# Kernel optimization log

Hardware: AMD Instinct MI355X
Metric: run time of the kernel (lower is better)

Reference implementation:

```python
import jax, jax.numpy as jnp
import numpy as np

BN_EPS = 1e-5

def _bn(x, gamma, beta):
    # BatchNorm1d in training mode: batch mean, biased variance
    m = jnp.mean(x, axis=0)
    v = jnp.var(x, axis=0)
    return (x - m) * jax.lax.rsqrt(v + BN_EPS) * gamma + beta

def setup_inputs() -> dict:
    key = jax.random.key(0)
    ks = jax.random.split(key, 12)
    N, E, D, ED = 50000, 600000, 128, 16
    s = lambda k, sh: jax.random.normal(k, sh, dtype=jnp.float32) * 0.05
    return {
        'h': jax.random.normal(ks[0], (N, D), dtype=jnp.float32),
        'edge_index': jax.random.randint(ks[1], (2, E), 0, N, dtype=jnp.int64),
        'edge_attr': jax.random.normal(ks[2], (E, ED), dtype=jnp.float32),
        'ee_w1': s(ks[3], (ED, D)), 'ee_b1': jnp.zeros((D,), jnp.float32),
        'ee_g1': jnp.ones((D,), jnp.float32), 'ee_bb1': jnp.zeros((D,), jnp.float32),
        'ee_w2': s(ks[4], (D, D)), 'ee_b2': jnp.zeros((D,), jnp.float32),
        'mlp_w1': s(ks[5], (D, D)), 'mlp_b1': jnp.zeros((D,), jnp.float32),
        'mlp_g1': jnp.ones((D,), jnp.float32), 'mlp_bb1': jnp.zeros((D,), jnp.float32),
        'mlp_w2': s(ks[6], (D, D)), 'mlp_b2': jnp.zeros((D,), jnp.float32),
        'mlp_g2': jnp.ones((D,), jnp.float32), 'mlp_bb2': jnp.zeros((D,), jnp.float32),
    }

def reference(h, edge_index, edge_attr, ee_w1, ee_b1, ee_g1, ee_bb1, ee_w2, ee_b2,
              mlp_w1, mlp_b1, mlp_g1, mlp_bb1, mlp_w2, mlp_b2, mlp_g2, mlp_bb2):
    N = h.shape[0]
    src, dst = edge_index[0], edge_index[1]
    # edge_encoder: Linear -> BN -> ReLU -> Linear
    e = jax.nn.relu(_bn(edge_attr @ ee_w1 + ee_b1, ee_g1, ee_bb1)) @ ee_w2 + ee_b2  # [E, D]
    # scatter-add edge embeddings to destination nodes
    agg_edge = jax.ops.segment_sum(e, dst, num_segments=N)  # [N, D]
    h = h + agg_edge
    # GINConv (eps=0): mlp(h + sum_{j->i} h_j)
    neigh = jax.ops.segment_sum(h[src], dst, num_segments=N)  # [N, D]
    z = h + neigh
    z = jax.nn.relu(_bn(z @ mlp_w1 + mlp_b1, mlp_g1, mlp_bb1))
    z = jax.nn.relu(_bn(z @ mlp_w2 + mlp_b2, mlp_g2, mlp_bb2))
    return z
```

## Files before the change

kernel.cpp:

```cpp
#include <hip/hip_runtime.h>
#include <hip/hip_bf16.h>

#define DD 128
#define EDIM 16
#define WPB 4
#define PSE 68
#define NCOPY 16
#define PREP_TB 208
#define PREP_AM 1024
#define PREP_HI 1024

typedef short v8s __attribute__((ext_vector_type(8)));
typedef float v4f __attribute__((ext_vector_type(4)));

__device__ __forceinline__ float ldf(const void* p, int i, int bf){
  return bf ? __bfloat162float(((const __hip_bfloat16*)p)[i])
            : ((const float*)p)[i];
}
__device__ __forceinline__ float bfu_lo(unsigned u){
  unsigned b = (u & 0xffffu) << 16; float f; __builtin_memcpy(&f,&b,4); return f;
}
__device__ __forceinline__ float bfu_hi(unsigned u){
  unsigned b = u & 0xffff0000u; float f; __builtin_memcpy(&f,&b,4); return f;
}
__device__ __forceinline__ unsigned short f2bf(float f){
  unsigned u; __builtin_memcpy(&u,&f,4);
  unsigned r = (u + 0x7fffu + ((u>>16)&1u)) >> 16;
  return (unsigned short)r;
}
__device__ __forceinline__ unsigned packbf(float a, float b){
  return (unsigned)f2bf(a) | ((unsigned)f2bf(b) << 16);
}

__global__ void k_detect(const void* g1, const int* ei, int E, int* flags){
  __shared__ int nz;
  if (threadIdx.x==0) nz = 0;
  __syncthreads();
  long long total = 2LL*E;
  long long stride = (total/1024) & ~1LL;
  if (stride < 2) stride = 2;
  long long idx = (long long)threadIdx.x*stride + 1;
  if (idx < total && ei[idx] != 0) atomicAdd(&nz, 1);
  __syncthreads();
  if (threadIdx.x==0){
    unsigned w = *(const unsigned*)g1;
    flags[0] = (w == 0x3F803F80u) ? 1 : 0;
    flags[1] = (nz == 0) ? 1 : 0;
  }
}

__global__ __launch_bounds__(256) void k_prep(
    const void* w0, const void* w1, const void* w2, const void* we1,
    const void* __restrict__ attr, const int* __restrict__ ei, int E,
    const int* __restrict__ flags, short* __restrict__ Bt,
    float* __restrict__ Ssum, float* __restrict__ csum, int* __restrict__ deg)
{
  const int b = blockIdx.x;
  const int t = threadIdx.x;
  if (b < PREP_TB){
    const int bf = flags[0];
    for (int idx = b*256 + t; idx < 3*16384 + 2048; idx += PREP_TB*256){
      if (idx < 3*16384){
        int m = idx >> 14, r = idx & 16383;
        int nn = r >> 7, k = r & 127;
        const void* w = (m==0) ? w0 : ((m==1) ? w1 : w2);
        Bt[idx] = (short)f2bf(ldf(w, k*DD + nn, bf));
      } else {
        int r = idx - 3*16384;
        int nn = r >> 4, k = r & 15;
        Bt[idx] = (short)f2bf(ldf(we1, k*DD + nn, bf));
      }
    }
    return;
  }
  if (b < PREP_TB + PREP_AM){
    const int rb = b - PREP_TB;
    __shared__ short Ws[4*512];
    __shared__ float sred[4][256];
    __shared__ float credu[4][16];
    const int wv = t >> 6, lane = t & 63, l15 = lane & 15, quad = lane >> 4;
    const int bf = flags[0];
    const int el = lane >> 1, half = lane & 1;
    short* W = &Ws[wv*512];

    v4f acc = (v4f){0.f,0.f,0.f,0.f};
    float cs[8];
    #pragma unroll
    for (int j=0;j<8;++j) cs[j]=0.f;

    const int nchunks = (E + 31) >> 5;
    for (int c = rb*4 + wv; c < nchunks; c += PREP_AM*4){
      const int e = c*32 + el;
      const bool ok = (e < E);
      float f[8];
      if (bf){
        uint4 u = {0u,0u,0u,0u};
        if (ok) u = reinterpret_cast<const uint4*>(attr)[(size_t)e*2 + half];
        f[0]=bfu_lo(u.x); f[1]=bfu_hi(u.x); f[2]=bfu_lo(u.y); f[3]=bfu_hi(u.y);
        f[4]=bfu_lo(u.z); f[5]=bfu_hi(u.z); f[6]=bfu_lo(u.w); f[7]=bfu_hi(u.w);
      } else {
        float4 v0 = {0,0,0,0}, v1 = {0,0,0,0};
        if (ok){
          const float4* ap = reinterpret_cast<const float4*>(attr) +
                             (size_t)e*4 + half*2;
          v0 = ap[0]; v1 = ap[1];
        }
        f[0]=v0.x; f[1]=v0.y; f[2]=v0.z; f[3]=v0.w;
        f[4]=v1.x; f[5]=v1.y; f[6]=v1.z; f[7]=v1.w;
      }
      #pragma unroll
      for (int j=0;j<8;++j){
        cs[j] += f[j];
        W[(half*8 + j)*32 + el] = (short)f2bf(f[j]);
      }
      v8s a = *reinterpret_cast<const v8s*>(&W[l15*32 + quad*8]);
      acc = __builtin_amdgcn_mfma_f32_16x16x32_bf16(a, a, acc, 0,0,0);
    }

    #pragma unroll
    for (int r=0;r<4;++r) sred[wv][(quad*4 + r)*16 + l15] = acc[r];
    #pragma unroll
    for (int j=0;j<8;++j){
      #pragma unroll
      for (int off=2; off<64; off<<=1) cs[j] += __shfl_xor(cs[j], off, 64);
    }
    if (lane < 2){
      #pragma unroll
      for (int j=0;j<8;++j) credu[wv][lane*8 + j] = cs[j];
    }
    __syncthreads();
    const int cp = rb & (NCOPY-1);
    float s = sred[0][t]+sred[1][t]+sred[2][t]+sred[3][t];
    atomicAdd(&Ssum[cp*256 + t], s);
    if (t < 16){
      float s2 = credu[0][t]+credu[1][t]+credu[2][t]+credu[3][t];
      atomicAdd(&csum[cp*16 + t], s2);
    }
    return;
  }
  {
    const int rb = b - (PREP_TB + PREP_AM);
    const int i64 = flags[1];
    const int2* ei2 = (const int2*)ei;
    for (int e = rb*256 + t; e < E; e += PREP_HI*256){
      int d = i64 ? ei2[E + e].x : ei[E + e];
      atomicAdd(&deg[d], 1);
    }
  }
}

__global__ __launch_bounds__(256) void k_scan_pe(
    const int* __restrict__ deg, int n, int nb,
    const void* __restrict__ w1, const void* __restrict__ g,
    const void* __restrict__ bb,
    const float* __restrict__ Ssum, const float* __restrict__ csum,
    float Einv, const int* __restrict__ flags,
    float* __restrict__ sc, float* __restrict__ sh,
    int* __restrict__ bsum)
{
  const int t = threadIdx.x;
  if ((int)blockIdx.x == nb){
    __shared__ float fS[256];
    __shared__ float fc[16];
    const int bf = flags[0];
    {
      float a0 = 0.f;
      #pragma unroll
      for (int c=0;c<NCOPY;++c) a0 += Ssum[c*256 + t];
      fS[t] = a0;
      if (t < 16){
        float a2 = 0.f;
        #pragma unroll
        for (int c=0;c<NCOPY;++c) a2 += csum[c*16 + t];
        fc[t] = a2;
      }
    }
    __syncthreads();
    if (t < 128){
      const int j = t;
      float w[EDIM];
      #pragma unroll
      for (int p=0;p<EDIM;++p) w[p] = ldf(w1, p*DD + j, bf);
      float mu0 = 0.f;
      #pragma unroll
      for (int p=0;p<EDIM;++p) mu0 += fc[p]*Einv*w[p];
      float s2 = 0.f;
      #pragma unroll
      for (int p=0;p<EDIM;++p){
        float acc = 0.f;
        #pragma unroll
        for (int q=0;q<EDIM;++q) acc += fS[p*16 + q]*w[q];
        s2 += w[p]*acc;
      }
      float var = s2*Einv - mu0*mu0;
      float scv = ldf(g, j, bf) * rsqrtf(var + 1e-5f);
      sc[j] = scv;
      sh[j] = ldf(bb, j, bf) - mu0*scv;
    }
    return;
  }
  __shared__ int red[256];
  const int base = blockIdx.x*1024;
  int s = 0;
  for (int i = t; i < 1024; i += 256){
    int gi = base + i;
    s += (gi < n) ? deg[gi] : 0;
  }
  red[t] = s; __syncthreads();
  for (int off=128; off>0; off>>=1){
    if (t < off) red[t] += red[t+off];
    __syncthreads();
  }
  if (t==0) bsum[blockIdx.x] = red[0];
}

__global__ void k_scan_final(const int* __restrict__ deg, int n, int nwin, int nb,
                             const int* __restrict__ bsum,
                             int* __restrict__ offsets, int* __restrict__ cursor,
                             int* __restrict__ win2node){
  __shared__ int red[256];
  __shared__ int pre[2];
  const int t = threadIdx.x;
  {
    int v = (t < nb) ? bsum[t] : 0;
    red[t] = v; __syncthreads();
    for (int off=1; off<256; off<<=1){
      int x = (t>=off) ? red[t-off] : 0;
      __syncthreads();
      red[t] += x; __syncthreads();
    }
    if (t == (int)blockIdx.x) pre[0] = red[t] - v;
    if (t == 255) pre[1] = red[255];
    __syncthreads();
  }
  const int base = blockIdx.x*1024 + t*4;
  int v4[4]; int s = 0;
  #pragma unroll
  for (int k=0;k<4;++k){
    int gi = base + k;
    v4[k] = (gi < n) ? deg[gi] : 0;
    s += v4[k];
  }
  red[t] = s; __syncthreads();
  for (int off=1; off<256; off<<=1){
    int x = (t>=off) ? red[t-off] : 0;
    __syncthreads();
    red[t] += x; __syncthreads();
  }
  int ex = pre[0] + red[t] - s;
  #pragma unroll
  for (int k=0;k<4;++k){
    int gi = base + k;
    if (gi < n){
      offsets[gi] = ex; cursor[gi] = ex;
      int end = ex + v4[k];
      for (int w = (ex + 63) >> 6; (w << 6) < end; ++w) win2node[w] = gi;
    }
    ex += v4[k];
  }
  if (blockIdx.x==0 && t==0){
    offsets[n] = pre[1];
    win2node[nwin] = n - 1;
  }
}

__global__ void k_scatter(const int* __restrict__ ei, int E,
                          const int* __restrict__ flags,
                          int* __restrict__ cursor, int2* __restrict__ se){
  const int i64 = flags[1];
  const int2* ei2 = (const int2*)ei;
  for (int e = blockIdx.x*blockDim.x + threadIdx.x; e < E;
       e += gridDim.x*blockDim.x){
    int d = i64 ? ei2[E + e].x : ei[E + e];
    int s = i64 ? ei2[e].x     : ei[e];
    int pp = atomicAdd(&cursor[d], 1);
    se[pp] = make_int2(s, e);
  }
}

__global__ __launch_bounds__(256) void k_edgeagg(
    const void* __restrict__ attr, const int2* __restrict__ se,
    const short* __restrict__ w1t,
    const float* __restrict__ sc, const float* __restrict__ sh,
    const int* __restrict__ offsets, const int* __restrict__ win2node,
    const int* __restrict__ flags, int n, int E, float* __restrict__ Pagg)
{
  __shared__ __align__(16) float Ps[DD*PSE];
  const int t = threadIdx.x;
  const int wv = t >> 6, lane = t & 63, l15 = lane & 15, quad = lane >> 4;
  const int bf = flags[0];
  const int G0 = blockIdx.x * (64*WPB);
  if (G0 >= E) return;

  const int4 w2nv = *reinterpret_cast<const int4*>(&win2node[blockIdx.x*WPB]);
  const int w2na[4] = {w2nv.x, w2nv.y, w2nv.z, w2nv.w};
  const int w2next = win2node[blockIdx.x*WPB + WPB];

  v8s afrag[WPB];
  #pragma unroll
  for (int w=0; w<WPB; ++w){
    afrag[w] = (v8s){0,0,0,0,0,0,0,0};
    if (quad < 2){
      int slot = G0 + w*64 + wv*16 + l15;
      if (slot < E){
        int e = se[slot].y;
        if (bf){
          afrag[w] = *reinterpret_cast<const v8s*>(
                (const short*)attr + (size_t)e*EDIM + quad*8);
        } else {
          const float4* ap = reinterpret_cast<const float4*>(
                (const float*)attr + (size_t)e*EDIM + quad*8);
          float4 v0 = ap[0], v1 = ap[1];
          v8s av;
          av[0]=(short)f2bf(v0.x); av[1]=(short)f2bf(v0.y);
          av[2]=(short)f2bf(v0.z); av[3]=(short)f2bf(v0.w);
          av[4]=(short)f2bf(v1.x); av[5]=(short)f2bf(v1.y);
          av[6]=(short)f2bf(v1.z); av[7]=(short)f2bf(v1.w);
          afrag[w] = av;
        }
      }
    }
  }

  v8s bfrag[8];
  #pragma unroll
  for (int cg=0;cg<8;++cg){
    bfrag[cg] = (v8s){0,0,0,0,0,0,0,0};
    if (quad < 2)
      bfrag[cg] = *reinterpret_cast<const v8s*>(&w1t[(cg*16+l15)*EDIM + quad*8]);
  }
  const float scA = sc[lane],      shA = sh[lane];
  const float scB = sc[lane + 64], shB = sh[lane + 64];

  #pragma unroll
  for (int w=0; w<WPB; ++w){
    const int B0 = G0 + w*64;
    if (B0 >= E) break;
    const int Bend = (B0 + 64 < E) ? (B0 + 64) : E;

    #pragma unroll
    for (int cg=0;cg<8;++cg){
      v4f acc = (v4f){0.f,0.f,0.f,0.f};
      acc = __builtin_amdgcn_mfma_f32_16x16x32_bf16(bfrag[cg], afrag[w], acc, 0,0,0);
      #pragma unroll
      for (int reg=0;reg<4;++reg)
        Ps[(cg*16 + quad*4 + reg)*PSE + wv*16 + l15] = acc[reg];
    }
    __syncthreads();

    const int i1 = (w < WPB-1) ? w2na[w+1] : w2next;
    int idx = w2na[w] + wv;
    int nb = 0, ne = 0;
    if (idx <= i1){ nb = offsets[idx]; ne = offsets[idx+1]; }
    while (idx <= i1){
      const int idxn = idx + 4;
      int nbn = 0, nen = 0;
      if (idxn <= i1){ nbn = offsets[idxn]; nen = offsets[idxn+1]; }
      int s0 = nb - B0; if (s0 < 0) s0 = 0;
      const int s1 = (ne < Bend ? ne : Bend) - B0;
      if (s1 > s0){
        float sa = 0.f, sb = 0.f;
        const int c1 = (s1 - 1) >> 2;
        for (int cc = s0 >> 2; cc <= c1; ++cc){
          v4f va = *reinterpret_cast<const v4f*>(&Ps[lane*PSE + cc*4]);
          v4f vb = *reinterpret_cast<const v4f*>(&Ps[(lane+64)*PSE + cc*4]);
          #pragma unroll
          for (int k2=0;k2<4;++k2){
            const int r = cc*4 + k2;
            if (r >= s0 && r < s1){
              sa += fmaxf(fmaf(va[k2], scA, shA), 0.f);
              sb += fmaxf(fmaf(vb[k2], scB, shB), 0.f);
            }
          }
        }
        if (nb < B0 || ne > Bend){
          atomicAdd(&Pagg[(size_t)idx*DD + lane], sa);
          atomicAdd(&Pagg[(size_t)idx*DD + lane + 64], sb);
        } else {
          Pagg[(size_t)idx*DD + lane] = sa;
          Pagg[(size_t)idx*DD + lane + 64] = sb;
        }
      }
      nb = nbn; ne = nen; idx = idxn;
    }
    __syncthreads();
  }
}

__global__ __launch_bounds__(256) void k_gather_z(
    const uint4* __restrict__ hnew16, const int* __restrict__ offsets,
    const int2* __restrict__ se, int n, uint4* __restrict__ zH16)
{
  const int wv = threadIdx.x >> 6, lane = threadIdx.x & 63;
  const int g = lane >> 4, c16 = lane & 15;
  for (int i = blockIdx.x*4 + wv; i < n; i += gridDim.x*4){
    const int beg = offsets[i], end = offsets[i+1];
    float a0=0.f,a1=0.f,a2=0.f,a3=0.f,a4=0.f,a5=0.f,a6=0.f,a7=0.f;
    int c0 = beg;
    for (; c0 + 8 <= end; c0 += 8){
      int s1 = se[c0 + g].x;
      int s2 = se[c0 + 4 + g].x;
      uint4 u = hnew16[(size_t)s1*16 + c16];
      uint4 v = hnew16[(size_t)s2*16 + c16];
      a0 += bfu_lo(u.x)+bfu_lo(v.x); a1 += bfu_hi(u.x)+bfu_hi(v.x);
      a2 += bfu_lo(u.y)+bfu_lo(v.y); a3 += bfu_hi(u.y)+bfu_hi(v.y);
      a4 += bfu_lo(u.z)+bfu_lo(v.z); a5 += bfu_hi(u.z)+bfu_hi(v.z);
      a6 += bfu_lo(u.w)+bfu_lo(v.w); a7 += bfu_hi(u.w)+bfu_hi(v.w);
    }
    for (; c0 < end; c0 += 4){
      int r = c0 + g;
      if (r < end){
        uint4 u = hnew16[(size_t)se[r].x*16 + c16];
        a0 += bfu_lo(u.x); a1 += bfu_hi(u.x);
        a2 += bfu_lo(u.y); a3 += bfu_hi(u.y);
        a4 += bfu_lo(u.z); a5 += bfu_hi(u.z);
        a6 += bfu_lo(u.w); a7 += bfu_hi(u.w);
      }
    }
    a0 += __shfl_xor(a0,16,64); a1 += __shfl_xor(a1,16,64);
    a2 += __shfl_xor(a2,16,64); a3 += __shfl_xor(a3,16,64);
    a4 += __shfl_xor(a4,16,64); a5 += __shfl_xor(a5,16,64);
    a6 += __shfl_xor(a6,16,64); a7 += __shfl_xor(a7,16,64);
    a0 += __shfl_xor(a0,32,64); a1 += __shfl_xor(a1,32,64);
    a2 += __shfl_xor(a2,32,64); a3 += __shfl_xor(a3,32,64);
    a4 += __shfl_xor(a4,32,64); a5 += __shfl_xor(a5,32,64);
    a6 += __shfl_xor(a6,32,64); a7 += __shfl_xor(a7,32,64);
    if (lane < 16){
      uint4 m = hnew16[(size_t)i*16 + lane];
      uint4 o;
      o.x = packbf(a0+bfu_lo(m.x), a1+bfu_hi(m.x));
      o.y = packbf(a2+bfu_lo(m.y), a3+bfu_hi(m.y));
      o.z = packbf(a4+bfu_lo(m.z), a5+bfu_hi(m.z));
      o.w = packbf(a6+bfu_lo(m.w), a7+bfu_hi(m.w));
      zH16[(size_t)i*16 + lane] = o;
    }
  }
}

__global__ __launch_bounds__(256) void k_gemm_mfma(
    const short* __restrict__ A, const float* __restrict__ Af32,
    const short* __restrict__ Bt, const void* __restrict__ bias,
    const float* __restrict__ bnstats, const void* __restrict__ bng,
    const void* __restrict__ bnbb, float bninv,
    const int* __restrict__ deg, const void* __restrict__ H,
    const int* __restrict__ flags, int n,
    __hip_bfloat16* __restrict__ out, float* __restrict__ stats, int mode)
{
  __shared__ float sb[256];
  __shared__ float sbn[256];
  const int t = threadIdx.x;
  const int bfi = flags[0];
  sb[t] = 0.f;
  if (bnstats && t < 128){
    float mean = bnstats[t]*bninv;
    float var  = bnstats[DD+t]*bninv - mean*mean;
    float s = ldf(bng, t, bfi) * rsqrtf(var + 1e-5f);
    sbn[t] = s;
    sbn[128+t] = ldf(bnbb, t, bfi) - mean*s;
  }
  __syncthreads();
  const int wv = t >> 6, lane = t & 63, l15 = lane & 15, quad = lane >> 4;
  const int R0 = blockIdx.x*64 + wv*16;

  v8s a[4];
  {
    const int arow = R0 + l15;
    const bool ok = (arow < n);
    #pragma unroll
    for (int ks=0;ks<4;++ks){
      const int k0 = ks*32 + quad*8;
      float f[8];
      if (Af32){
        float4 v0 = {0,0,0,0}, v1 = {0,0,0,0};
        if (ok){
          const float4* ap = reinterpret_cast<const float4*>(
              Af32 + (size_t)arow*DD + k0);
          v0 = ap[0]; v1 = ap[1];
        }
        f[0]=v0.x; f[1]=v0.y; f[2]=v0.z; f[3]=v0.w;
        f[4]=v1.x; f[5]=v1.y; f[6]=v1.z; f[7]=v1.w;
        v8s av;
        #pragma unroll
        for (int j=0;j<8;++j) av[j] = (short)f2bf(f[j]);
        a[ks] = av;
      } else {
        uint4 u = {0u,0u,0u,0u};
        if (ok) u = *reinterpret_cast<const uint4*>(&A[(size_t)arow*DD + k0]);
        if (bnstats){
          f[0]=bfu_lo(u.x); f[1]=bfu_hi(u.x); f[2]=bfu_lo(u.y); f[3]=bfu_hi(u.y);
          f[4]=bfu_lo(u.z); f[5]=bfu_hi(u.z); f[6]=bfu_lo(u.w); f[7]=bfu_hi(u.w);
          v8s av;
          #pragma unroll
          for (int j=0;j<8;++j)
            av[j] = (short)f2bf(fmaxf(fmaf(f[j], sbn[k0+j], sbn[128+k0+j]), 0.f));
          a[ks] = av;
        } else {
          a[ks] = *reinterpret_cast<v8s*>(&u);
        }
      }
    }
  }

  v4f acc[8];
  #pragma unroll
  for (int cg=0;cg<8;++cg) acc[cg] = (v4f){0.f,0.f,0.f,0.f};
  #pragma unroll
  for (int ks=0;ks<4;++ks){
    #pragma unroll
    for (int cg=0;cg<8;++cg){
      v8s b = *reinterpret_cast<const v8s*>(
                &Bt[(cg*16+l15)*DD + ks*32 + quad*8]);
      acc[cg] = __builtin_amdgcn_mfma_f32_16x16x32_bf16(a[ks], b, acc[cg], 0,0,0);
    }
  }

  float bc[8];
  #pragma unroll
  for (int cg=0;cg<8;++cg) bc[cg] = ldf(bias, cg*16 + l15, bfi);
  float ss[8], sq[8];
  #pragma unroll
  for (int cg=0;cg<8;++cg){ ss[cg]=0.f; sq[cg]=0.f; }

  #pragma unroll
  for (int reg=0;reg<4;++reg){
    const int row = R0 + quad*4 + reg;
    if (row < n){
      float degf = (mode==1) ? (float)deg[row] : 0.f;
      #pragma unroll
      for (int cg=0;cg<8;++cg){
        const int col = cg*16 + l15;
        float x = acc[cg][reg];
        if (mode==1) x = fmaf(degf, bc[cg], x) + ldf(H, (size_t)row*DD + col, bfi);
        else         x += bc[cg];
        out[(size_t)row*DD + col] = __float2bfloat16(x);
        ss[cg] += x; sq[cg] += x*x;
      }
    }
  }

  if (stats){
    #pragma unroll
    for (int cg=0;cg<8;++cg){
      float s = ss[cg], q = sq[cg];
      s += __shfl_xor(s, 16, 64); s += __shfl_xor(s, 32, 64);
      q += __shfl_xor(q, 16, 64); q += __shfl_xor(q, 32, 64);
      if (quad == 0){
        atomicAdd(&sb[cg*16 + l15], s);
        atomicAdd(&sb[128 + cg*16 + l15], q);
      }
    }
    __syncthreads();
    atomicAdd(&stats[t], sb[t]);
  }
}

__global__ void k_final(const unsigned* __restrict__ yH,
                        const float* __restrict__ bnstats,
                        const void* __restrict__ bng, const void* __restrict__ bnbb,
                        float bninv, int n, const int* __restrict__ flags,
                        void* __restrict__ out){
  __shared__ float sck[128], shk[128];
  const int bf = flags[0];
  const int t = threadIdx.x;
  if (t < 128){
    float mean = bnstats[t]*bninv;
    float var  = bnstats[DD+t]*bninv - mean*mean;
    float s = ldf(bng, t, bf) * rsqrtf(var + 1e-5f);
    sck[t] = s;
    shk[t] = ldf(bnbb, t, bf) - mean*s;
  }
  __syncthreads();
  const int nw = n*64;
  for (int i = blockIdx.x*blockDim.x + t; i < nw;
       i += gridDim.x*blockDim.x){
    const int j0 = (i & 63)*2;
    unsigned u = yH[i];
    float v0 = fmaxf(fmaf(bfu_lo(u), sck[j0],   shk[j0]),   0.f);
    float v1 = fmaxf(fmaf(bfu_hi(u), sck[j0+1], shk[j0+1]), 0.f);
    if (bf){
      ((unsigned*)out)[i] = packbf(v0, v1);
    } else {
      *reinterpret_cast<float2*>((float*)out + 2*(size_t)i) = make_float2(v0, v1);
    }
  }
}

extern "C" void kernel_launch(void* const* d_in, const int* in_sizes, int n_in,
                              void* d_out, int out_size, void* d_ws, size_t ws_size,
                              hipStream_t stream)
{
  const void* h       = d_in[0];
  const int*  ei      = (const int*)d_in[1];
  const void* attr    = d_in[2];
  const void* ee_w1   = d_in[3];
  const void* ee_g1   = d_in[5];
  const void* ee_bb1  = d_in[6];
  const void* ee_w2   = d_in[7];
  const void* ee_b2   = d_in[8];
  const void* mlp_w1  = d_in[9];
  const void* mlp_b1  = d_in[10];
  const void* mlp_g1  = d_in[11];
  const void* mlp_bb1 = d_in[12];
  const void* mlp_w2  = d_in[13];
  const void* mlp_b2  = d_in[14];
  const void* mlp_g2  = d_in[15];
  const void* mlp_bb2 = d_in[16];

  const int N = in_sizes[0] / DD;
  const int E = in_sizes[1] / 2;
  const int nb = (N + 1023) / 1024;
  const int e64  = (E + 63) / 64;
  const int e256 = (E + 64*WPB - 1) / (64*WPB);

  char* p = (char*)d_ws;
  auto alloc = [&](size_t bytes)->char*{
    char* r = p;
    p += (bytes + 255) & ~size_t(255);
    return r;
  };
  int* flags = (int*)alloc(8);
  char* zbase = p;
  int*   deg    = (int*)  zbase;
  float* csum   = (float*)(zbase + (size_t)N*4);
  float* Ssum   = (float*)(zbase + (size_t)N*4 + 1024);
  float* stats1 = (float*)(zbase + (size_t)N*4 + 1024 + 16384);
  float* stats2 = (float*)(zbase + (size_t)N*4 + 1024 + 16384 + 1024);
  float* Pagg   = (float*)(zbase + (size_t)N*4 + 1024 + 16384 + 2048);
  size_t zlen   = (size_t)N*4 + 1024 + 16384 + 2048 + (size_t)N*DD*4;
  p += (zlen + 255) & ~size_t(255);
  int*   bsum     = (int*)  alloc(256*4);
  int*   offsets  = (int*)  alloc((size_t)(N+1)*4);
  int*   cursor   = (int*)  alloc((size_t)N*4);
  int*   win2node = (int*)  alloc((size_t)(e64 + 8)*4);
  int2*  se       = (int2*) alloc((size_t)E*8);
  short* Bt      = (short*)alloc((size_t)(3*DD*DD + DD*EDIM)*2);
  short* w1t     = Bt + 3*DD*DD;
  float* ebn_sc  = (float*)alloc(512);
  float* ebn_sh  = (float*)alloc(512);
  short* hnewH   = (short*)alloc((size_t)N*DD*2);
  short* zH      = (short*)alloc((size_t)N*DD*2);
  short* y1H     = (short*)alloc((size_t)N*DD*2);
  short* y2H     = (short*)alloc((size_t)N*DD*2);
  (void)ws_size; (void)n_in; (void)out_size;

  const int g64  = (N + 63) / 64;
  const int gseg = (N + 15) / 16;

  hipMemsetAsync(zbase, 0, zlen, stream);
  k_detect<<<1, 1024, 0, stream>>>(ee_g1, ei, E, flags);
  k_prep<<<PREP_TB + PREP_AM + PREP_HI, 256, 0, stream>>>(
      ee_w2, mlp_w1, mlp_w2, ee_w1, attr, ei, E, flags, Bt, Ssum, csum, deg);
  k_scan_pe<<<nb + 1, 256, 0, stream>>>(deg, N, nb, ee_w1, ee_g1, ee_bb1,
                                        Ssum, csum, 1.0f/(float)E, flags,
                                        ebn_sc, ebn_sh, bsum);
  k_scan_final<<<nb, 256, 0, stream>>>(deg, N, e64, nb, bsum, offsets, cursor,
                                       win2node);
  k_scatter<<<1024, 256, 0, stream>>>(ei, E, flags, cursor, se);

  k_edgeagg<<<e256, 256, 0, stream>>>(attr, se, w1t, ebn_sc, ebn_sh,
                                      offsets, win2node, flags, N, E, Pagg);

  k_gemm_mfma<<<g64, 256, 0, stream>>>(nullptr, Pagg, Bt, ee_b2,
                                       nullptr, nullptr, nullptr, 0.f,
                                       deg, h, flags, N,
                                       (__hip_bfloat16*)hnewH, nullptr, 1);
  k_gather_z<<<gseg, 256, 0, stream>>>((const uint4*)hnewH, offsets, se, N,
                                       (uint4*)zH);
  k_gemm_mfma<<<g64, 256, 0, stream>>>(zH, nullptr, Bt + 16384, mlp_b1,
                                       nullptr, nullptr, nullptr, 0.f,
                                       nullptr, nullptr, flags, N,
                                       (__hip_bfloat16*)y1H, stats1, 0);
  k_gemm_mfma<<<g64, 256, 0, stream>>>(y1H, nullptr, Bt + 32768, mlp_b2,
                                       stats1, mlp_g1, mlp_bb1, 1.0f/(float)N,
                                       nullptr, nullptr, flags, N,
                                       (__hip_bfloat16*)y2H, stats2, 0);
  k_final<<<2048, 256, 0, stream>>>((const unsigned*)y2H, stats2,
                                    mlp_g2, mlp_bb2, 1.0f/(float)N,
                                    N, flags, d_out);
}
```

Measured before the change: 400.6 us.

## Merge pipeline stages into two persistent cooperative kernels with grid syncs

Each stage becomes a device function. The front half (detect, prep, scan, scatter, edge aggregation) and the back half (GEMMs, gather, final BN) each run inside one cooperative persistent kernel, with grid-wide barriers between phases. The grid is sized from occupancy queries, and the old multi-kernel path is kept as a fallback. This removes about a dozen kernel launches and their launch gaps. The cost is grid-sync overhead, fewer resident blocks per phase, and lower per-phase parallelism than the original grid sizes.

```diff
diff --git a/kernel.cpp b/kernel.cpp
--- a/kernel.cpp
+++ b/kernel.cpp
@@ -1,14 +1,14 @@
 #include <hip/hip_runtime.h>
 #include <hip/hip_bf16.h>
+#include <hip/hip_cooperative_groups.h>
+
+namespace cg = cooperative_groups;
 
 #define DD 128
 #define EDIM 16
 #define WPB 4
 #define PSE 68
 #define NCOPY 16
-#define PREP_TB 208
-#define PREP_AM 1024
-#define PREP_HI 1024
 
 typedef short v8s __attribute__((ext_vector_type(8)));
 typedef float v4f __attribute__((ext_vector_type(4)));
@@ -32,175 +32,128 @@
   return (unsigned)f2bf(a) | ((unsigned)f2bf(b) << 16);
 }
 
-__global__ void k_detect(const void* g1, const int* ei, int E, int* flags){
+
+__device__ void ph_detect(const void* g1, const int* ei, int E, int* flags){
   __shared__ int nz;
-  if (threadIdx.x==0) nz = 0;
+  const int t = threadIdx.x;
+  if (t==0) nz = 0;
   __syncthreads();
   long long total = 2LL*E;
   long long stride = (total/1024) & ~1LL;
   if (stride < 2) stride = 2;
-  long long idx = (long long)threadIdx.x*stride + 1;
-  if (idx < total && ei[idx] != 0) atomicAdd(&nz, 1);
-  __syncthreads();
-  if (threadIdx.x==0){
+  int cnt = 0;
+  #pragma unroll
+  for (int k=0;k<4;++k){
+    long long idx = (long long)(t + 256*k)*stride + 1;
+    if (idx < total && ei[idx] != 0) cnt++;
+  }
+  if (cnt) atomicAdd(&nz, cnt);
+  __syncthreads();
+  if (t==0){
     unsigned w = *(const unsigned*)g1;
     flags[0] = (w == 0x3F803F80u) ? 1 : 0;
     flags[1] = (nz == 0) ? 1 : 0;
   }
 }
 
-__global__ __launch_bounds__(256) void k_prep(
-    const void* w0, const void* w1, const void* w2, const void* we1,
-    const void* __restrict__ attr, const int* __restrict__ ei, int E,
-    const int* __restrict__ flags, short* __restrict__ Bt,
-    float* __restrict__ Ssum, float* __restrict__ csum, int* __restrict__ deg)
-{
-  const int b = blockIdx.x;
+__device__ void ph_transB(int rk, int cnt, const void* w0, const void* w1,
+                          const void* w2, const void* we1, int bf,
+                          short* __restrict__ Bt){
+  for (int idx = rk*256 + (int)threadIdx.x; idx < 3*16384 + 2048; idx += cnt*256){
+    if (idx < 3*16384){
+      int m = idx >> 14, r = idx & 16383;
+      int nn = r >> 7, k = r & 127;
+      const void* w = (m==0) ? w0 : ((m==1) ? w1 : w2);
+      Bt[idx] = (short)f2bf(ldf(w, k*DD + nn, bf));
+    } else {
+      int r = idx - 3*16384;
+      int nn = r >> 4, k = r & 15;
+      Bt[idx] = (short)f2bf(ldf(we1, k*DD + nn, bf));
+    }
+  }
+}
+
+__device__ void ph_moments(int rk, int cnt, const void* __restrict__ attr, int E,
+                           int bf, float* __restrict__ Ssum,
+                           float* __restrict__ csum, char* sm){
+  short* Ws   = (short*)sm;
+  float* sred = (float*)(sm + 4096);
+  float* credu= (float*)(sm + 8192);
   const int t = threadIdx.x;
-  if (b < PREP_TB){
-    const int bf = flags[0];
-    for (int idx = b*256 + t; idx < 3*16384 + 2048; idx += PREP_TB*256){
-      if (idx < 3*16384){
-        int m = idx >> 14, r = idx & 16383;
-        int nn = r >> 7, k = r & 127;
-        const void* w = (m==0) ? w0 : ((m==1) ? w1 : w2);
-        Bt[idx] = (short)f2bf(ldf(w, k*DD + nn, bf));
-      } else {
-        int r = idx - 3*16384;
-        int nn = r >> 4, k = r & 15;
-        Bt[idx] = (short)f2bf(ldf(we1, k*DD + nn, bf));
+  const int wv = t >> 6, lane = t & 63, l15 = lane & 15, quad = lane >> 4;
+  const int el = lane >> 1, half = lane & 1;
+  short* W = &Ws[wv*512];
+
+  v4f acc = (v4f){0.f,0.f,0.f,0.f};
+  float cs[8];
+  #pragma unroll
+  for (int j=0;j<8;++j) cs[j]=0.f;
+
+  const int nchunks = (E + 31) >> 5;
+  for (int c = rk*4 + wv; c < nchunks; c += cnt*4){
+    const int e = c*32 + el;
+    const bool ok = (e < E);
+    float f[8];
+    if (bf){
+      uint4 u = {0u,0u,0u,0u};
+      if (ok) u = reinterpret_cast<const uint4*>(attr)[(size_t)e*2 + half];
+      f[0]=bfu_lo(u.x); f[1]=bfu_hi(u.x); f[2]=bfu_lo(u.y); f[3]=bfu_hi(u.y);
+      f[4]=bfu_lo(u.z); f[5]=bfu_hi(u.z); f[6]=bfu_lo(u.w); f[7]=bfu_hi(u.w);
+    } else {
+      float4 v0 = {0,0,0,0}, v1 = {0,0,0,0};
+      if (ok){
+        const float4* ap = reinterpret_cast<const float4*>(attr) +
+                           (size_t)e*4 + half*2;
+        v0 = ap[0]; v1 = ap[1];
       }
-    }
-    return;
-  }
-  if (b < PREP_TB + PREP_AM){
-    const int rb = b - PREP_TB;
-    __shared__ short Ws[4*512];
-    __shared__ float sred[4][256];
-    __shared__ float credu[4][16];
-    const int wv = t >> 6, lane = t & 63, l15 = lane & 15, quad = lane >> 4;
-    const int bf = flags[0];
-    const int el = lane >> 1, half = lane & 1;
-    short* W = &Ws[wv*512];
-
-    v4f acc = (v4f){0.f,0.f,0.f,0.f};
-    float cs[8];
-    #pragma unroll
-    for (int j=0;j<8;++j) cs[j]=0.f;
-
-    const int nchunks = (E + 31) >> 5;
-    for (int c = rb*4 + wv; c < nchunks; c += PREP_AM*4){
-      const int e = c*32 + el;
-      const bool ok = (e < E);
-      float f[8];
-      if (bf){
-        uint4 u = {0u,0u,0u,0u};
-        if (ok) u = reinterpret_cast<const uint4*>(attr)[(size_t)e*2 + half];
-        f[0]=bfu_lo(u.x); f[1]=bfu_hi(u.x); f[2]=bfu_lo(u.y); f[3]=bfu_hi(u.y);
-        f[4]=bfu_lo(u.z); f[5]=bfu_hi(u.z); f[6]=bfu_lo(u.w); f[7]=bfu_hi(u.w);
-      } else {
-        float4 v0 = {0,0,0,0}, v1 = {0,0,0,0};
-        if (ok){
-          const float4* ap = reinterpret_cast<const float4*>(attr) +
-                             (size_t)e*4 + half*2;
-          v0 = ap[0]; v1 = ap[1];
-        }
-        f[0]=v0.x; f[1]=v0.y; f[2]=v0.z; f[3]=v0.w;
-        f[4]=v1.x; f[5]=v1.y; f[6]=v1.z; f[7]=v1.w;
-      }
-      #pragma unroll
-      for (int j=0;j<8;++j){
-        cs[j] += f[j];
-        W[(half*8 + j)*32 + el] = (short)f2bf(f[j]);
-      }
-      v8s a = *reinterpret_cast<const v8s*>(&W[l15*32 + quad*8]);
-      acc = __builtin_amdgcn_mfma_f32_16x16x32_bf16(a, a, acc, 0,0,0);
-    }
-
-    #pragma unroll
-    for (int r=0;r<4;++r) sred[wv][(quad*4 + r)*16 + l15] = acc[r];
+      f[0]=v0.x; f[1]=v0.y; f[2]=v0.z; f[3]=v0.w;
+      f[4]=v1.x; f[5]=v1.y; f[6]=v1.z; f[7]=v1.w;
+    }
     #pragma unroll
     for (int j=0;j<8;++j){
-      #pragma unroll
-      for (int off=2; off<64; off<<=1) cs[j] += __shfl_xor(cs[j], off, 64);
-    }
-    if (lane < 2){
-      #pragma unroll
-      for (int j=0;j<8;++j) credu[wv][lane*8 + j] = cs[j];
-    }
-    __syncthreads();
-    const int cp = rb & (NCOPY-1);
-    float s = sred[0][t]+sred[1][t]+sred[2][t]+sred[3][t];
-    atomicAdd(&Ssum[cp*256 + t], s);
-    if (t < 16){
-      float s2 = credu[0][t]+credu[1][t]+credu[2][t]+credu[3][t];
-      atomicAdd(&csum[cp*16 + t], s2);
-    }
-    return;
-  }
-  {
-    const int rb = b - (PREP_TB + PREP_AM);
-    const int i64 = flags[1];
-    const int2* ei2 = (const int2*)ei;
-    for (int e = rb*256 + t; e < E; e += PREP_HI*256){
-      int d = i64 ? ei2[E + e].x : ei[E + e];
-      atomicAdd(&deg[d], 1);
-    }
-  }
-}
-
-__global__ __launch_bounds__(256) void k_scan_pe(
-    const int* __restrict__ deg, int n, int nb,
-    const void* __restrict__ w1, const void* __restrict__ g,
-    const void* __restrict__ bb,
-    const float* __restrict__ Ssum, const float* __restrict__ csum,
-    float Einv, const int* __restrict__ flags,
-    float* __restrict__ sc, float* __restrict__ sh,
-    int* __restrict__ bsum)
-{
+      cs[j] += f[j];
+      W[(half*8 + j)*32 + el] = (short)f2bf(f[j]);
+    }
+    v8s a = *reinterpret_cast<const v8s*>(&W[l15*32 + quad*8]);
+    acc = __builtin_amdgcn_mfma_f32_16x16x32_bf16(a, a, acc, 0,0,0);
+  }
+
+  #pragma unroll
+  for (int r=0;r<4;++r) sred[wv*256 + (quad*4 + r)*16 + l15] = acc[r];
+  #pragma unroll
+  for (int j=0;j<8;++j){
+    #pragma unroll
+    for (int off=2; off<64; off<<=1) cs[j] += __shfl_xor(cs[j], off, 64);
+  }
+  if (lane < 2){
+    #pragma unroll
+    for (int j=0;j<8;++j) credu[wv*16 + lane*8 + j] = cs[j];
+  }
+  __syncthreads();
+  const int cp = rk & (NCOPY-1);
+  float s = sred[t]+sred[256+t]+sred[512+t]+sred[768+t];
+  atomicAdd(&Ssum[cp*256 + t], s);
+  if (t < 16){
+    float s2 = credu[t]+credu[16+t]+credu[32+t]+credu[48+t];
+    atomicAdd(&csum[cp*16 + t], s2);
+  }
+  __syncthreads();
+}
+
+__device__ void ph_hist(int rk, int cnt, const int* __restrict__ ei, int E,
+                        int i64, int* __restrict__ deg){
+  const int2* ei2 = (const int2*)ei;
+  for (int e = rk*256 + (int)threadIdx.x; e < E; e += cnt*256){
+    int d = i64 ? ei2[E + e].x : ei[E + e];
+    atomicAdd(&deg[d], 1);
+  }
+}
+
+__device__ void ph_scanpartial(int b, const int* __restrict__ deg, int n,
+                               int* __restrict__ bsum, char* sm){
+  int* red = (int*)sm;
   const int t = threadIdx.x;
-  if ((int)blockIdx.x == nb){
-    __shared__ float fS[256];
-    __shared__ float fc[16];
-    const int bf = flags[0];
-    {
-      float a0 = 0.f;
-      #pragma unroll
-      for (int c=0;c<NCOPY;++c) a0 += Ssum[c*256 + t];
-      fS[t] = a0;
-      if (t < 16){
-        float a2 = 0.f;
-        #pragma unroll
-        for (int c=0;c<NCOPY;++c) a2 += csum[c*16 + t];
-        fc[t] = a2;
-      }
-    }
-    __syncthreads();
-    if (t < 128){
-      const int j = t;
-      float w[EDIM];
-      #pragma unroll
-      for (int p=0;p<EDIM;++p) w[p] = ldf(w1, p*DD + j, bf);
-      float mu0 = 0.f;
-      #pragma unroll
-      for (int p=0;p<EDIM;++p) mu0 += fc[p]*Einv*w[p];
-      float s2 = 0.f;
-      #pragma unroll
-      for (int p=0;p<EDIM;++p){
-        float acc = 0.f;
-        #pragma unroll
-        for (int q=0;q<EDIM;++q) acc += fS[p*16 + q]*w[q];
-        s2 += w[p]*acc;
-      }
-      float var = s2*Einv - mu0*mu0;
-      float scv = ldf(g, j, bf) * rsqrtf(var + 1e-5f);
-      sc[j] = scv;
-      sh[j] = ldf(bb, j, bf) - mu0*scv;
-    }
-    return;
-  }
-  __shared__ int red[256];
-  const int base = blockIdx.x*1024;
+  const int base = b*1024;
   int s = 0;
   for (int i = t; i < 1024; i += 256){
     int gi = base + i;
@@ -211,15 +164,63 @@
     if (t < off) red[t] += red[t+off];
     __syncthreads();
   }
-  if (t==0) bsum[blockIdx.x] = red[0];
-}
-
-__global__ void k_scan_final(const int* __restrict__ deg, int n, int nwin, int nb,
-                             const int* __restrict__ bsum,
+  if (t==0) bsum[b] = red[0];
+  __syncthreads();
+}
+
+__device__ void ph_edgebn(const void* __restrict__ w1, const void* __restrict__ g,
+                          const void* __restrict__ bb,
+                          const float* __restrict__ Ssum,
+                          const float* __restrict__ csum,
+                          float Einv, int bf,
+                          float* __restrict__ sc, float* __restrict__ sh,
+                          char* sm){
+  float* fS = (float*)sm;
+  float* fc = (float*)(sm + 1024);
+  const int t = threadIdx.x;
+  {
+    float a0 = 0.f;
+    #pragma unroll
+    for (int c=0;c<NCOPY;++c) a0 += Ssum[c*256 + t];
+    fS[t] = a0;
+    if (t < 16){
+      float a2 = 0.f;
+      #pragma unroll
+      for (int c=0;c<NCOPY;++c) a2 += csum[c*16 + t];
+      fc[t] = a2;
+    }
+  }
+  __syncthreads();
+  if (t < 128){
+    const int j = t;
+    float w[EDIM];
+    #pragma unroll
+    for (int p=0;p<EDIM;++p) w[p] = ldf(w1, p*DD + j, bf);
+    float mu0 = 0.f;
+    #pragma unroll
+    for (int p=0;p<EDIM;++p) mu0 += fc[p]*Einv*w[p];
+    float s2 = 0.f;
+    #pragma unroll
+    for (int p=0;p<EDIM;++p){
+      float acc = 0.f;
+      #pragma unroll
+      for (int q=0;q<EDIM;++q) acc += fS[p*16 + q]*w[q];
+      s2 += w[p]*acc;
+    }
+    float var = s2*Einv - mu0*mu0;
+    float scv = ldf(g, j, bf) * rsqrtf(var + 1e-5f);
+    sc[j] = scv;
+    sh[j] = ldf(bb, j, bf) - mu0*scv;
+  }
+  __syncthreads();
+}
+
+__device__ void ph_scanfinal(int b, const int* __restrict__ deg, int n, int nwin,
+                             int nb, const int* __restrict__ bsum,
                              int* __restrict__ offsets, int* __restrict__ cursor,
-                             int* __restrict__ win2node){
-  __shared__ int red[256];
-  __shared__ int pre[2];
+                             int* __restrict__ win2node, char* sm){
+  int* red = (int*)sm;
+  int* pre = (int*)(sm + 1024);
   const int t = threadIdx.x;
   {
     int v = (t < nb) ? bsum[t] : 0;
@@ -229,17 +230,17 @@
       __syncthreads();
       red[t] += x; __syncthreads();
     }
-    if (t == (int)blockIdx.x) pre[0] = red[t] - v;
+    if (t == b) pre[0] = red[t] - v;
     if (t == 255) pre[1] = red[255];
     __syncthreads();
   }
-  const int base = blockIdx.x*1024 + t*4;
-  int v4[4]; int s = 0;
+  const int base = b*1024 + t*4;
+  int v4a[4]; int s = 0;
   #pragma unroll
   for (int k=0;k<4;++k){
     int gi = base + k;
-    v4[k] = (gi < n) ? deg[gi] : 0;
-    s += v4[k];
+    v4a[k] = (gi < n) ? deg[gi] : 0;
+    s += v4a[k];
   }
   red[t] = s; __syncthreads();
   for (int off=1; off<256; off<<=1){
@@ -253,24 +254,23 @@
     int gi = base + k;
     if (gi < n){
       offsets[gi] = ex; cursor[gi] = ex;
-      int end = ex + v4[k];
+      int end = ex + v4a[k];
       for (int w = (ex + 63) >> 6; (w << 6) < end; ++w) win2node[w] = gi;
     }
-    ex += v4[k];
-  }
-  if (blockIdx.x==0 && t==0){
+    ex += v4a[k];
+  }
+  if (b==0 && t==0){
     offsets[n] = pre[1];
     win2node[nwin] = n - 1;
   }
-}
-
-__global__ void k_scatter(const int* __restrict__ ei, int E,
-                          const int* __restrict__ flags,
-                          int* __restrict__ cursor, int2* __restrict__ se){
-  const int i64 = flags[1];
+  __syncthreads();
+}
+
+__device__ void ph_scatter(int rk, int cnt, const int* __restrict__ ei, int E,
+                           int i64, int* __restrict__ cursor,
+                           int2* __restrict__ se){
   const int2* ei2 = (const int2*)ei;
-  for (int e = blockIdx.x*blockDim.x + threadIdx.x; e < E;
-       e += gridDim.x*blockDim.x){
+  for (int e = rk*256 + (int)threadIdx.x; e < E; e += cnt*256){
     int d = i64 ? ei2[E + e].x : ei[E + e];
     int s = i64 ? ei2[e].x     : ei[e];
     int pp = atomicAdd(&cursor[d], 1);
@@ -278,23 +278,21 @@
   }
 }
 
-__global__ __launch_bounds__(256) void k_edgeagg(
-    const void* __restrict__ attr, const int2* __restrict__ se,
-    const short* __restrict__ w1t,
-    const float* __restrict__ sc, const float* __restrict__ sh,
-    const int* __restrict__ offsets, const int* __restrict__ win2node,
-    const int* __restrict__ flags, int n, int E, float* __restrict__ Pagg)
-{
-  __shared__ __align__(16) float Ps[DD*PSE];
+__device__ void ph_edgeagg(int tile, const void* __restrict__ attr,
+                           const int2* __restrict__ se,
+                           const short* __restrict__ w1t,
+                           const float* __restrict__ sc, const float* __restrict__ sh,
+                           const int* __restrict__ offsets,
+                           const int* __restrict__ win2node,
+                           int bf, int n, int E, float* __restrict__ Pagg,
+                           float* Ps){
   const int t = threadIdx.x;
   const int wv = t >> 6, lane = t & 63, l15 = lane & 15, quad = lane >> 4;
-  const int bf = flags[0];
-  const int G0 = blockIdx.x * (64*WPB);
-  if (G0 >= E) return;
-
-  const int4 w2nv = *reinterpret_cast<const int4*>(&win2node[blockIdx.x*WPB]);
+  const int G0 = tile * (64*WPB);
+
+  const int4 w2nv = *reinterpret_cast<const int4*>(&win2node[tile*WPB]);
   const int w2na[4] = {w2nv.x, w2nv.y, w2nv.z, w2nv.w};
-  const int w2next = win2node[blockIdx.x*WPB + WPB];
+  const int w2next = win2node[tile*WPB + WPB];
 
   v8s afrag[WPB];
   #pragma unroll
@@ -324,10 +322,10 @@
 
   v8s bfrag[8];
   #pragma unroll
-  for (int cg=0;cg<8;++cg){
-    bfrag[cg] = (v8s){0,0,0,0,0,0,0,0};
+  for (int cg2=0;cg2<8;++cg2){
+    bfrag[cg2] = (v8s){0,0,0,0,0,0,0,0};
     if (quad < 2)
-      bfrag[cg] = *reinterpret_cast<const v8s*>(&w1t[(cg*16+l15)*EDIM + quad*8]);
+      bfrag[cg2] = *reinterpret_cast<const v8s*>(&w1t[(cg2*16+l15)*EDIM + quad*8]);
   }
   const float scA = sc[lane],      shA = sh[lane];
   const float scB = sc[lane + 64], shB = sh[lane + 64];
@@ -339,27 +337,27 @@
     const int Bend = (B0 + 64 < E) ? (B0 + 64) : E;
 
     #pragma unroll
-    for (int cg=0;cg<8;++cg){
+    for (int cg2=0;cg2<8;++cg2){
       v4f acc = (v4f){0.f,0.f,0.f,0.f};
-      acc = __builtin_amdgcn_mfma_f32_16x16x32_bf16(bfrag[cg], afrag[w], acc, 0,0,0);
+      acc = __builtin_amdgcn_mfma_f32_16x16x32_bf16(bfrag[cg2], afrag[w], acc, 0,0,0);
       #pragma unroll
       for (int reg=0;reg<4;++reg)
-        Ps[(cg*16 + quad*4 + reg)*PSE + wv*16 + l15] = acc[reg];
+        Ps[(cg2*16 + quad*4 + reg)*PSE + wv*16 + l15] = acc[reg];
     }
     __syncthreads();
 
     const int i1 = (w < WPB-1) ? w2na[w+1] : w2next;
     int idx = w2na[w] + wv;
-    int nb = 0, ne = 0;
-    if (idx <= i1){ nb = offsets[idx]; ne = offsets[idx+1]; }
+    int nbv = 0, nev = 0;
+    if (idx <= i1){ nbv = offsets[idx]; nev = offsets[idx+1]; }
     while (idx <= i1){
       const int idxn = idx + 4;
       int nbn = 0, nen = 0;
       if (idxn <= i1){ nbn = offsets[idxn]; nen = offsets[idxn+1]; }
-      int s0 = nb - B0; if (s0 < 0) s0 = 0;
-      const int s1 = (ne < Bend ? ne : Bend) - B0;
+      int s0 = nbv - B0; if (s0 < 0) s0 = 0;
+      const int s1 = (nev < Bend ? nev : Bend) - B0;
       if (s1 > s0){
-        float sa = 0.f, sb = 0.f;
+        float sa = 0.f, sb2 = 0.f;
         const int c1 = (s1 - 1) >> 2;
         for (int cc = s0 >> 2; cc <= c1; ++cc){
           v4f va = *reinterpret_cast<const v4f*>(&Ps[lane*PSE + cc*4]);
@@ -368,88 +366,82 @@
           for (int k2=0;k2<4;++k2){
             const int r = cc*4 + k2;
             if (r >= s0 && r < s1){
-              sa += fmaxf(fmaf(va[k2], scA, shA), 0.f);
-              sb += fmaxf(fmaf(vb[k2], scB, shB), 0.f);
+              sa  += fmaxf(fmaf(va[k2], scA, shA), 0.f);
+              sb2 += fmaxf(fmaf(vb[k2], scB, shB), 0.f);
             }
           }
         }
-        if (nb < B0 || ne > Bend){
+        if (nbv < B0 || nev > Bend){
           atomicAdd(&Pagg[(size_t)idx*DD + lane], sa);
-          atomicAdd(&Pagg[(size_t)idx*DD + lane + 64], sb);
+          atomicAdd(&Pagg[(size_t)idx*DD + lane + 64], sb2);
         } else {
           Pagg[(size_t)idx*DD + lane] = sa;
-          Pagg[(size_t)idx*DD + lane + 64] = sb;
+          Pagg[(size_t)idx*DD + lane + 64] = sb2;
         }
       }
-      nb = nbn; ne = nen; idx = idxn;
+      nbv = nbn; nev = nen; idx = idxn;
     }
     __syncthreads();
   }
 }
 
-__global__ __launch_bounds__(256) void k_gather_z(
-    const uint4* __restrict__ hnew16, const int* __restrict__ offsets,
-    const int2* __restrict__ se, int n, uint4* __restrict__ zH16)
-{
-  const int wv = threadIdx.x >> 6, lane = threadIdx.x & 63;
+__device__ void ph_gather(int i, const uint4* __restrict__ hnew16,
+                          const int* __restrict__ offsets,
+                          const int2* __restrict__ se, uint4* __restrict__ zH16){
+  const int lane = threadIdx.x & 63;
   const int g = lane >> 4, c16 = lane & 15;
-  for (int i = blockIdx.x*4 + wv; i < n; i += gridDim.x*4){
-    const int beg = offsets[i], end = offsets[i+1];
-    float a0=0.f,a1=0.f,a2=0.f,a3=0.f,a4=0.f,a5=0.f,a6=0.f,a7=0.f;
-    int c0 = beg;
-    for (; c0 + 8 <= end; c0 += 8){
-      int s1 = se[c0 + g].x;
-      int s2 = se[c0 + 4 + g].x;
-      uint4 u = hnew16[(size_t)s1*16 + c16];
-      uint4 v = hnew16[(size_t)s2*16 + c16];
-      a0 += bfu_lo(u.x)+bfu_lo(v.x); a1 += bfu_hi(u.x)+bfu_hi(v.x);
-      a2 += bfu_lo(u.y)+bfu_lo(v.y); a3 += bfu_hi(u.y)+bfu_hi(v.y);
-      a4 += bfu_lo(u.z)+bfu_lo(v.z); a5 += bfu_hi(u.z)+bfu_hi(v.z);
-      a6 += bfu_lo(u.w)+bfu_lo(v.w); a7 += bfu_hi(u.w)+bfu_hi(v.w);
-    }
-    for (; c0 < end; c0 += 4){
-      int r = c0 + g;
-      if (r < end){
-        uint4 u = hnew16[(size_t)se[r].x*16 + c16];
-        a0 += bfu_lo(u.x); a1 += bfu_hi(u.x);
-        a2 += bfu_lo(u.y); a3 += bfu_hi(u.y);
-        a4 += bfu_lo(u.z); a5 += bfu_hi(u.z);
-        a6 += bfu_lo(u.w); a7 += bfu_hi(u.w);
-      }
-    }
-    a0 += __shfl_xor(a0,16,64); a1 += __shfl_xor(a1,16,64);
-    a2 += __shfl_xor(a2,16,64); a3 += __shfl_xor(a3,16,64);
-    a4 += __shfl_xor(a4,16,64); a5 += __shfl_xor(a5,16,64);
-    a6 += __shfl_xor(a6,16,64); a7 += __shfl_xor(a7,16,64);
-    a0 += __shfl_xor(a0,32,64); a1 += __shfl_xor(a1,32,64);
-    a2 += __shfl_xor(a2,32,64); a3 += __shfl_xor(a3,32,64);
-    a4 += __shfl_xor(a4,32,64); a5 += __shfl_xor(a5,32,64);
-    a6 += __shfl_xor(a6,32,64); a7 += __shfl_xor(a7,32,64);
-    if (lane < 16){
-      uint4 m = hnew16[(size_t)i*16 + lane];
-      uint4 o;
-      o.x = packbf(a0+bfu_lo(m.x), a1+bfu_hi(m.x));
-      o.y = packbf(a2+bfu_lo(m.y), a3+bfu_hi(m.y));
-      o.z = packbf(a4+bfu_lo(m.z), a5+bfu_hi(m.z));
-      o.w = packbf(a6+bfu_lo(m.w), a7+bfu_hi(m.w));
-      zH16[(size_t)i*16 + lane] = o;
-    }
-  }
-}
-
-__global__ __launch_bounds__(256) void k_gemm_mfma(
-    const short* __restrict__ A, const float* __restrict__ Af32,
-    const short* __restrict__ Bt, const void* __restrict__ bias,
-    const float* __restrict__ bnstats, const void* __restrict__ bng,
-    const void* __restrict__ bnbb, float bninv,
-    const int* __restrict__ deg, const void* __restrict__ H,
-    const int* __restrict__ flags, int n,
-    __hip_bfloat16* __restrict__ out, float* __restrict__ stats, int mode)
-{
-  __shared__ float sb[256];
-  __shared__ float sbn[256];
+  const int beg = offsets[i], end = offsets[i+1];
+  float a0=0.f,a1=0.f,a2=0.f,a3=0.f,a4=0.f,a5=0.f,a6=0.f,a7=0.f;
+  int c0 = beg;
+  for (; c0 + 8 <= end; c0 += 8){
+    int s1 = se[c0 + g].x;
+    int s2 = se[c0 + 4 + g].x;
+    uint4 u = hnew16[(size_t)s1*16 + c16];
+    uint4 v = hnew16[(size_t)s2*16 + c16];
+    a0 += bfu_lo(u.x)+bfu_lo(v.x); a1 += bfu_hi(u.x)+bfu_hi(v.x);
+    a2 += bfu_lo(u.y)+bfu_lo(v.y); a3 += bfu_hi(u.y)+bfu_hi(v.y);
+    a4 += bfu_lo(u.z)+bfu_lo(v.z); a5 += bfu_hi(u.z)+bfu_hi(v.z);
+    a6 += bfu_lo(u.w)+bfu_lo(v.w); a7 += bfu_hi(u.w)+bfu_hi(v.w);
+  }
+  for (; c0 < end; c0 += 4){
+    int r = c0 + g;
+    if (r < end){
+      uint4 u = hnew16[(size_t)se[r].x*16 + c16];
+      a0 += bfu_lo(u.x); a1 += bfu_hi(u.x);
+      a2 += bfu_lo(u.y); a3 += bfu_hi(u.y);
+      a4 += bfu_lo(u.z); a5 += bfu_hi(u.z);
+      a6 += bfu_lo(u.w); a7 += bfu_hi(u.w);
+    }
+  }
+  a0 += __shfl_xor(a0,16,64); a1 += __shfl_xor(a1,16,64);
+  a2 += __shfl_xor(a2,16,64); a3 += __shfl_xor(a3,16,64);
+  a4 += __shfl_xor(a4,16,64); a5 += __shfl_xor(a5,16,64);
+  a6 += __shfl_xor(a6,16,64); a7 += __shfl_xor(a7,16,64);
+  a0 += __shfl_xor(a0,32,64); a1 += __shfl_xor(a1,32,64);
+  a2 += __shfl_xor(a2,32,64); a3 += __shfl_xor(a3,32,64);
+  a4 += __shfl_xor(a4,32,64); a5 += __shfl_xor(a5,32,64);
+  a6 += __shfl_xor(a6,32,64); a7 += __shfl_xor(a7,32,64);
+  if (lane < 16){
+    uint4 m = hnew16[(size_t)i*16 + lane];
+    uint4 o;
+    o.x = packbf(a0+bfu_lo(m.x), a1+bfu_hi(m.x));
+    o.y = packbf(a2+bfu_lo(m.y), a3+bfu_hi(m.y));
+    o.z = packbf(a4+bfu_lo(m.z), a5+bfu_hi(m.z));
+    o.w = packbf(a6+bfu_lo(m.w), a7+bfu_hi(m.w));
+    zH16[(size_t)i*16 + lane] = o;
+  }
+}
+
+__device__ void ph_gemm(int tile, const short* __restrict__ A,
+                        const float* __restrict__ Af32,
+                        const short* __restrict__ Bt, const void* __restrict__ bias,
+                        const float* __restrict__ bnstats, const void* __restrict__ bng,
+                        const void* __restrict__ bnbb, float bninv,
+                        const int* __restrict__ deg, const void* __restrict__ H,
+                        int bfi, int n, __hip_bfloat16* __restrict__ out,
+                        float* __restrict__ stats, int mode,
+                        float* sb, float* sbn){
   const int t = threadIdx.x;
-  const int bfi = flags[0];
   sb[t] = 0.f;
   if (bnstats && t < 128){
     float mean = bnstats[t]*bninv;
@@ -460,7 +452,7 @@
   }
   __syncthreads();
   const int wv = t >> 6, lane = t & 63, l15 = lane & 15, quad = lane >> 4;
-  const int R0 = blockIdx.x*64 + wv*16;
+  const int R0 = tile*64 + wv*16;
 
   v8s a[4];
   {
@@ -503,23 +495,23 @@
 
   v4f acc[8];
   #pragma unroll
-  for (int cg=0;cg<8;++cg) acc[cg] = (v4f){0.f,0.f,0.f,0.f};
+  for (int cg2=0;cg2<8;++cg2) acc[cg2] = (v4f){0.f,0.f,0.f,0.f};
   #pragma unroll
   for (int ks=0;ks<4;++ks){
     #pragma unroll
-    for (int cg=0;cg<8;++cg){
+    for (int cg2=0;cg2<8;++cg2){
       v8s b = *reinterpret_cast<const v8s*>(
-                &Bt[(cg*16+l15)*DD + ks*32 + quad*8]);
-      acc[cg] = __builtin_amdgcn_mfma_f32_16x16x32_bf16(a[ks], b, acc[cg], 0,0,0);
+                &Bt[(cg2*16+l15)*DD + ks*32 + quad*8]);
+      acc[cg2] = __builtin_amdgcn_mfma_f32_16x16x32_bf16(a[ks], b, acc[cg2], 0,0,0);
     }
   }
 
   float bc[8];
   #pragma unroll
-  for (int cg=0;cg<8;++cg) bc[cg] = ldf(bias, cg*16 + l15, bfi);
+  for (int cg2=0;cg2<8;++cg2) bc[cg2] = ldf(bias, cg2*16 + l15, bfi);
   float ss[8], sq[8];
   #pragma unroll
-  for (int cg=0;cg<8;++cg){ ss[cg]=0.f; sq[cg]=0.f; }
+  for (int cg2=0;cg2<8;++cg2){ ss[cg2]=0.f; sq[cg2]=0.f; }
 
   #pragma unroll
   for (int reg=0;reg<4;++reg){
@@ -527,40 +519,39 @@
     if (row < n){
       float degf = (mode==1) ? (float)deg[row] : 0.f;
       #pragma unroll
-      for (int cg=0;cg<8;++cg){
-        const int col = cg*16 + l15;
-        float x = acc[cg][reg];
-        if (mode==1) x = fmaf(degf, bc[cg], x) + ldf(H, (size_t)row*DD + col, bfi);
-        else         x += bc[cg];
+      for (int cg2=0;cg2<8;++cg2){
+        const int col = cg2*16 + l15;
+        float x = acc[cg2][reg];
+        if (mode==1) x = fmaf(degf, bc[cg2], x) + ldf(H, (size_t)row*DD + col, bfi);
+        else         x += bc[cg2];
         out[(size_t)row*DD + col] = __float2bfloat16(x);
-        ss[cg] += x; sq[cg] += x*x;
+        ss[cg2] += x; sq[cg2] += x*x;
       }
     }
   }
 
   if (stats){
     #pragma unroll
-    for (int cg=0;cg<8;++cg){
-      float s = ss[cg], q = sq[cg];
+    for (int cg2=0;cg2<8;++cg2){
+      float s = ss[cg2], q = sq[cg2];
       s += __shfl_xor(s, 16, 64); s += __shfl_xor(s, 32, 64);
       q += __shfl_xor(q, 16, 64); q += __shfl_xor(q, 32, 64);
       if (quad == 0){
-        atomicAdd(&sb[cg*16 + l15], s);
-        atomicAdd(&sb[128 + cg*16 + l15], q);
+        atomicAdd(&sb[cg2*16 + l15], s);
+        atomicAdd(&sb[128 + cg2*16 + l15], q);
       }
     }
     __syncthreads();
     atomicAdd(&stats[t], sb[t]);
   }
-}
-
-__global__ void k_final(const unsigned* __restrict__ yH,
-                        const float* __restrict__ bnstats,
-                        const void* __restrict__ bng, const void* __restrict__ bnbb,
-                        float bninv, int n, const int* __restrict__ flags,
-                        void* __restrict__ out){
-  __shared__ float sck[128], shk[128];
-  const int bf = flags[0];
+  __syncthreads();
+}
+
+__device__ void ph_final(int b, int nG, const unsigned* __restrict__ yH,
+                         const float* __restrict__ bnstats,
+                         const void* __restrict__ bng, const void* __restrict__ bnbb,
+                         float bninv, int n, int bf, void* __restrict__ out,
+                         float* sck, float* shk){
   const int t = threadIdx.x;
   if (t < 128){
     float mean = bnstats[t]*bninv;
@@ -571,8 +562,7 @@
   }
   __syncthreads();
   const int nw = n*64;
-  for (int i = blockIdx.x*blockDim.x + t; i < nw;
-       i += gridDim.x*blockDim.x){
+  for (int i = b*256 + t; i < nw; i += nG*256){
     const int j0 = (i & 63)*2;
     unsigned u = yH[i];
     float v0 = fmaxf(fmaf(bfu_lo(u), sck[j0],   shk[j0]),   0.f);
@@ -584,6 +574,188 @@
     }
   }
 }
+
+
+struct CoopA {
+  const void* attr; const int* ei;
+  const void* w0; const void* w1; const void* w2; const void* we1;
+  const void* g1; const void* bb1;
+  int E, N, nb, nwin, e256, GA;
+  float Einv;
+  int* flags; short* Bt; const short* w1t;
+  float* Ssum; float* csum; int* deg; int* bsum;
+  int* offsets; int* cursor; int* win2node; int2* se;
+  float* sc; float* sh; float* Pagg;
+};
+
+__global__ __launch_bounds__(256) void k_coopA(CoopA P){
+  __shared__ __align__(16) char sm[DD*PSE*4];
+  cg::grid_group grid = cg::this_grid();
+  const int b = blockIdx.x;
+
+  if (b == 0) ph_detect(P.g1, P.ei, P.E, P.flags);
+  __threadfence();
+  grid.sync();
+
+  const int bf = P.flags[0], i64 = P.flags[1];
+  {
+    const int TBn = 64, HIn = 256;
+    const int AMn = P.GA - TBn - HIn;
+    if (b < TBn)            ph_transB(b, TBn, P.w0, P.w1, P.w2, P.we1, bf, P.Bt);
+    else if (b < TBn+AMn)   ph_moments(b-TBn, AMn, P.attr, P.E, bf, P.Ssum, P.csum, sm);
+    else                    ph_hist(b-TBn-AMn, HIn, P.ei, P.E, i64, P.deg);
+  }
+  __threadfence();
+  grid.sync();
+
+  if (b < P.nb)        ph_scanpartial(b, P.deg, P.N, P.bsum, sm);
+  else if (b == P.nb)  ph_edgebn(P.we1, P.g1, P.bb1, P.Ssum, P.csum, P.Einv, bf,
+                                 P.sc, P.sh, sm);
+  __threadfence();
+  grid.sync();
+
+  if (b < P.nb) ph_scanfinal(b, P.deg, P.N, P.nwin, P.nb, P.bsum,
+                             P.offsets, P.cursor, P.win2node, sm);
+  __threadfence();
+  grid.sync();
+
+  ph_scatter(b, P.GA, P.ei, P.E, i64, P.cursor, P.se);
+  __threadfence();
+  grid.sync();
+
+  for (int tile = b; tile < P.e256; tile += P.GA)
+    ph_edgeagg(tile, P.attr, P.se, P.w1t, P.sc, P.sh, P.offsets, P.win2node,
+               bf, P.N, P.E, P.Pagg, (float*)sm);
+}
+
+struct CoopB {
+  const float* Pagg; const short* Bt;
+  const void* eb2; const void* mb1; const void* mb2;
+  const void* mg1; const void* mbb1; const void* mg2; const void* mbb2;
+  const void* h; const int* deg; const int* flags;
+  const int* offsets; const int2* se;
+  int N, g64, GB; float Ninv;
+  short* hnewH; short* zH; short* y1H; short* y2H;
+  float* stats1; float* stats2; void* out;
+};
+
+__global__ __launch_bounds__(256) void k_coopB(CoopB P){
+  __shared__ float sb[256];
+  __shared__ float sbn[256];
+  cg::grid_group grid = cg::this_grid();
+  const int b = blockIdx.x;
+  const int bf = P.flags[0];
+
+  for (int tile = b; tile < P.g64; tile += P.GB)
+    ph_gemm(tile, nullptr, P.Pagg, P.Bt, P.eb2, nullptr, nullptr, nullptr, 0.f,
+            P.deg, P.h, bf, P.N, (__hip_bfloat16*)P.hnewH, nullptr, 1, sb, sbn);
+  __threadfence();
+  grid.sync();
+
+  {
+    const int wv = threadIdx.x >> 6;
+    for (int i = b*4 + wv; i < P.N; i += P.GB*4)
+      ph_gather(i, (const uint4*)P.hnewH, P.offsets, P.se, (uint4*)P.zH);
+  }
+  __threadfence();
+  grid.sync();
+
+  for (int tile = b; tile < P.g64; tile += P.GB)
+    ph_gemm(tile, P.zH, nullptr, P.Bt + 16384, P.mb1, nullptr, nullptr, nullptr,
+            0.f, nullptr, nullptr, bf, P.N, (__hip_bfloat16*)P.y1H, P.stats1, 0,
+            sb, sbn);
+  __threadfence();
+  grid.sync();
+
+  for (int tile = b; tile < P.g64; tile += P.GB)
+    ph_gemm(tile, P.y1H, nullptr, P.Bt + 32768, P.mb2, P.stats1, P.mg1, P.mbb1,
+            P.Ninv, nullptr, nullptr, bf, P.N, (__hip_bfloat16*)P.y2H, P.stats2,
+            0, sb, sbn);
+  __threadfence();
+  grid.sync();
+
+  ph_final(b, P.GB, (const unsigned*)P.y2H, P.stats2, P.mg2, P.mbb2, P.Ninv,
+           P.N, bf, P.out, sb, sbn);
+}
+
+
+__global__ __launch_bounds__(256) void k_detectK(const void* g1, const int* ei,
+                                                 int E, int* flags){
+  ph_detect(g1, ei, E, flags);
+}
+
+__global__ __launch_bounds__(256) void k_prepK(
+    const void* w0, const void* w1, const void* w2, const void* we1,
+    const void* attr, const int* ei, int E, const int* flags,
+    short* Bt, float* Ssum, float* csum, int* deg, int TB, int AM){
+  __shared__ __align__(16) char sm[16384];
+  const int b = blockIdx.x;
+  const int bf = flags[0], i64 = flags[1];
+  if (b < TB)            ph_transB(b, TB, w0, w1, w2, we1, bf, Bt);
+  else if (b < TB+AM)    ph_moments(b-TB, AM, attr, E, bf, Ssum, csum, sm);
+  else                   ph_hist(b-TB-AM, (int)gridDim.x-TB-AM, ei, E, i64, deg);
+}
+
+__global__ __launch_bounds__(256) void k_scanpeK(
+    const int* deg, int n, int nb, const void* w1, const void* g, const void* bb,
+    const float* Ssum, const float* csum, float Einv, const int* flags,
+    float* sc, float* sh, int* bsum){
+  __shared__ __align__(16) char sm[2048];
+  if ((int)blockIdx.x == nb)
+    ph_edgebn(w1, g, bb, Ssum, csum, Einv, flags[0], sc, sh, sm);
+  else
+    ph_scanpartial(blockIdx.x, deg, n, bsum, sm);
+}
+
+__global__ __launch_bounds__(256) void k_scanfinalK(
+    const int* deg, int n, int nwin, int nb, const int* bsum,
+    int* offsets, int* cursor, int* win2node){
+  __shared__ __align__(16) char sm[2048];
+  ph_scanfinal(blockIdx.x, deg, n, nwin, nb, bsum, offsets, cursor, win2node, sm);
+}
+
+__global__ __launch_bounds__(256) void k_scatterK(const int* ei, int E,
+                                                  const int* flags, int* cursor,
+                                                  int2* se){
+  ph_scatter(blockIdx.x, gridDim.x, ei, E, flags[1], cursor, se);
+}
+
+__global__ __launch_bounds__(256) void k_edgeaggK(
+    const void* attr, const int2* se, const short* w1t,
+    const float* sc, const float* sh, const int* offsets, const int* win2node,
+    const int* flags, int n, int E, float* Pagg){
+  __shared__ __align__(16) float Ps[DD*PSE];
+  ph_edgeagg(blockIdx.x, attr, se, w1t, sc, sh, offsets, win2node,
+             flags[0], n, E, Pagg, Ps);
+}
+
+__global__ __launch_bounds__(256) void k_gemmK(
+    const short* A, const float* Af32, const short* Bt, const void* bias,
+    const float* bnstats, const void* bng, const void* bnbb, float bninv,
+    const int* deg, const void* H, const int* flags, int n,
+    __hip_bfloat16* out, float* stats, int mode){
+  __shared__ float sb[256];
+  __shared__ float sbn[256];
+  ph_gemm(blockIdx.x, A, Af32, Bt, bias, bnstats, bng, bnbb, bninv, deg, H,
+          flags[0], n, out, stats, mode, sb, sbn);
+}
+
+__global__ __launch_bounds__(256) void k_gatherK(
+    const uint4* hnew16, const int* offsets, const int2* se, int n,
+    uint4* zH16){
+  const int wv = threadIdx.x >> 6;
+  for (int i = blockIdx.x*4 + wv; i < n; i += gridDim.x*4)
+    ph_gather(i, hnew16, offsets, se, zH16);
+}
+
+__global__ __launch_bounds__(256) void k_finalK(
+    const unsigned* yH, const float* bnstats, const void* bng, const void* bnbb,
+    float bninv, int n, const int* flags, void* out){
+  __shared__ float sck[128], shk[128];
+  ph_final(blockIdx.x, gridDim.x, yH, bnstats, bng, bnbb, bninv, n, flags[0],
+           out, sck, shk);
+}
+
 
 extern "C" void kernel_launch(void* const* d_in, const int* in_sizes, int n_in,
                               void* d_out, int out_size, void* d_ws, size_t ws_size,
@@ -646,35 +818,91 @@
   const int g64  = (N + 63) / 64;
   const int gseg = (N + 15) / 16;
 
+  static int s_ncu = 0, s_occA = -2, s_occB = -2;
+  if (s_occA == -2){
+    int dev = 0;
+    hipDeviceProp_t prop;
+    if (hipGetDevice(&dev) == hipSuccess &&
+        hipGetDeviceProperties(&prop, dev) == hipSuccess)
+      s_ncu = prop.multiProcessorCount;
+    if (s_ncu <= 0) s_ncu = 256;
+    int oa = 0, ob = 0;
+    if (hipOccupancyMaxActiveBlocksPerMultiprocessor(&oa, k_coopA, 256, 0)
+        != hipSuccess) oa = 0;
+    if (hipOccupancyMaxActiveBlocksPerMultiprocessor(&ob, k_coopB, 256, 0)
+        != hipSuccess) ob = 0;
+    s_occA = oa; s_occB = ob;
+  }
+  int GA = s_occA * s_ncu; if (GA > 2048) GA = 2048;
+  int GB = s_occB * s_ncu; if (GB > 2048) GB = 2048;
+
   hipMemsetAsync(zbase, 0, zlen, stream);
-  k_detect<<<1, 1024, 0, stream>>>(ee_g1, ei, E, flags);
-  k_prep<<<PREP_TB + PREP_AM + PREP_HI, 256, 0, stream>>>(
-      ee_w2, mlp_w1, mlp_w2, ee_w1, attr, ei, E, flags, Bt, Ssum, csum, deg);
-  k_scan_pe<<<nb + 1, 256, 0, stream>>>(deg, N, nb, ee_w1, ee_g1, ee_bb1,
-                                        Ssum, csum, 1.0f/(float)E, flags,
-                                        ebn_sc, ebn_sh, bsum);
-  k_scan_final<<<nb, 256, 0, stream>>>(deg, N, e64, nb, bsum, offsets, cursor,
-                                       win2node);
-  k_scatter<<<1024, 256, 0, stream>>>(ei, E, flags, cursor, se);
-
-  k_edgeagg<<<e256, 256, 0, stream>>>(attr, se, w1t, ebn_sc, ebn_sh,
-                                      offsets, win2node, flags, N, E, Pagg);
-
-  k_gemm_mfma<<<g64, 256, 0, stream>>>(nullptr, Pagg, Bt, ee_b2,
-                                       nullptr, nullptr, nullptr, 0.f,
-                                       deg, h, flags, N,
-                                       (__hip_bfloat16*)hnewH, nullptr, 1);
-  k_gather_z<<<gseg, 256, 0, stream>>>((const uint4*)hnewH, offsets, se, N,
-                                       (uint4*)zH);
-  k_gemm_mfma<<<g64, 256, 0, stream>>>(zH, nullptr, Bt + 16384, mlp_b1,
-                                       nullptr, nullptr, nullptr, 0.f,
-                                       nullptr, nullptr, flags, N,
-                                       (__hip_bfloat16*)y1H, stats1, 0);
-  k_gemm_mfma<<<g64, 256, 0, stream>>>(y1H, nullptr, Bt + 32768, mlp_b2,
-                                       stats1, mlp_g1, mlp_bb1, 1.0f/(float)N,
-                                       nullptr, nullptr, flags, N,
-                                       (__hip_bfloat16*)y2H, stats2, 0);
-  k_final<<<2048, 256, 0, stream>>>((const unsigned*)y2H, stats2,
-                                    mlp_g2, mlp_bb2, 1.0f/(float)N,
-                                    N, flags, d_out);
-}
+
+  bool frontLegacy = (GA < 384);
+  if (!frontLegacy){
+    CoopA pa;
+    pa.attr = attr; pa.ei = ei;
+    pa.w0 = ee_w2; pa.w1 = mlp_w1; pa.w2 = mlp_w2; pa.we1 = ee_w1;
+    pa.g1 = ee_g1; pa.bb1 = ee_bb1;
+    pa.E = E; pa.N = N; pa.nb = nb; pa.nwin = e64; pa.e256 = e256; pa.GA = GA;
+    pa.Einv = 1.0f/(float)E;
+    pa.flags = flags; pa.Bt = Bt; pa.w1t = w1t;
+    pa.Ssum = Ssum; pa.csum = csum; pa.deg = deg; pa.bsum = bsum;
+    pa.offsets = offsets; pa.cursor = cursor; pa.win2node = win2node; pa.se = se;
+    pa.sc = ebn_sc; pa.sh = ebn_sh; pa.Pagg = Pagg;
+    void* ka[] = { &pa };
+    if (hipLaunchCooperativeKernel((const void*)k_coopA, dim3(GA), dim3(256),
+                                   ka, 0, stream) != hipSuccess)
+      frontLegacy = true;
+  }
+  if (frontLegacy){
+    k_detectK<<<1, 256, 0, stream>>>(ee_g1, ei, E, flags);
+    k_prepK<<<208 + 1024 + 1024, 256, 0, stream>>>(
+        ee_w2, mlp_w1, mlp_w2, ee_w1, attr, ei, E, flags, Bt, Ssum, csum, deg,
+        208, 1024);
+    k_scanpeK<<<nb + 1, 256, 0, stream>>>(deg, N, nb, ee_w1, ee_g1, ee_bb1,
+                                          Ssum, csum, 1.0f/(float)E, flags,
+                                          ebn_sc, ebn_sh, bsum);
+    k_scanfinalK<<<nb, 256, 0, stream>>>(deg, N, e64, nb, bsum, offsets,
+                                         cursor, win2node);
+    k_scatterK<<<1024, 256, 0, stream>>>(ei, E, flags, cursor, se);
+    k_edgeaggK<<<e256, 256, 0, stream>>>(attr, se, w1t, ebn_sc, ebn_sh,
+                                         offsets, win2node, flags, N, E, Pagg);
+  }
+
+  bool backLegacy = (GB < 256);
+  if (!backLegacy){
+    CoopB pb;
+    pb.Pagg = Pagg; pb.Bt = Bt;
+    pb.eb2 = ee_b2; pb.mb1 = mlp_b1; pb.mb2 = mlp_b2;
+    pb.mg1 = mlp_g1; pb.mbb1 = mlp_bb1; pb.mg2 = mlp_g2; pb.mbb2 = mlp_bb2;
+    pb.h = h; pb.deg = deg; pb.flags = flags;
+    pb.offsets = offsets; pb.se = se;
+    pb.N = N; pb.g64 = g64; pb.GB = GB; pb.Ninv = 1.0f/(float)N;
+    pb.hnewH = hnewH; pb.zH = zH; pb.y1H = y1H; pb.y2H = y2H;
+    pb.stats1 = stats1; pb.stats2 = stats2; pb.out = d_out;
+    void* kb[] = { &pb };
+    if (hipLaunchCooperativeKernel((const void*)k_coopB, dim3(GB), dim3(256),
+                                   kb, 0, stream) != hipSuccess)
+      backLegacy = true;
+  }
+  if (backLegacy){
+    k_gemmK<<<g64, 256, 0, stream>>>(nullptr, Pagg, Bt, ee_b2,
+                                     nullptr, nullptr, nullptr, 0.f,
+                                     deg, h, flags, N,
+                                     (__hip_bfloat16*)hnewH, nullptr, 1);
+    k_gatherK<<<gseg, 256, 0, stream>>>((const uint4*)hnewH, offsets, se, N,
+                                        (uint4*)zH);
+    k_gemmK<<<g64, 256, 0, stream>>>(zH, nullptr, Bt + 16384, mlp_b1,
+                                     nullptr, nullptr, nullptr, 0.f,
+                                     nullptr, nullptr, flags, N,
+                                     (__hip_bfloat16*)y1H, stats1, 0);
+    k_gemmK<<<g64, 256, 0, stream>>>(y1H, nullptr, Bt + 32768, mlp_b2,
+                                     stats1, mlp_g1, mlp_bb1, 1.0f/(float)N,
+                                     nullptr, nullptr, flags, N,
+                                     (__hip_bfloat16*)y2H, stats2, 0);
+    k_finalK<<<2048, 256, 0, stream>>>((const unsigned*)y2H, stats2,
+                                       mlp_g2, mlp_bb2, 1.0f/(float)N,
+                                       N, flags, d_out);
+  }
+}
```

New measurement: 813.0 us. +102.9%, slower.
